# Optimization experiments

Measured on AMD Instinct MI355X. Metric: run time of the kernel, lower is better.

The kernel has to match this reference:

```python
import jax, jax.numpy as jnp
import numpy as np

SIZES = [128, 64, 32, 16, 8]   # H=W per pyramid level
REFINE = 2                     # gather/refine level -> 32x32
C = 256
GROUPS = 32                    # dim_out // 8
EPS = 1e-5


def _maxpool(x, k):
    # exact adaptive_max_pool2d when input size is divisible by output size
    if k == 1:
        return x
    return jax.lax.reduce_window(x, -jnp.inf, jax.lax.max,
                                 (1, 1, k, k), (1, 1, k, k), 'VALID')


def _upsample(x, f):
    # nearest-neighbor interpolate with exact integer scale factor
    if f == 1:
        return x
    return jnp.repeat(jnp.repeat(x, f, axis=2), f, axis=3)


def _conv1x1(x, w, b):
    return jnp.einsum('nchw,oc->nohw', x, w) + b[None, :, None, None]


def _group_norm(x, gamma, beta):
    n, c, h, w = x.shape
    xg = x.reshape(n, GROUPS, c // GROUPS, h, w)
    mu = xg.mean(axis=(2, 3, 4), keepdims=True)
    var = xg.var(axis=(2, 3, 4), keepdims=True)
    xg = (xg - mu) * jax.lax.rsqrt(var + EPS)
    return xg.reshape(n, c, h, w) * gamma[None, :, None, None] + beta[None, :, None, None]


def _nonlocal(x, g_w, g_b, th_w, th_b, ph_w, ph_b, out_w, out_b, gn_g, gn_b):
    n, c, h, w = x.shape
    N = h * w
    g_x = _conv1x1(x, g_w, g_b).reshape(n, c, N)       # [n,c,N]
    th_x = _conv1x1(x, th_w, th_b).reshape(n, c, N)
    ph_x = _conv1x1(x, ph_w, ph_b).reshape(n, c, N)
    # pairwise = theta^T @ phi / N  (dot_product mode, no softmax)
    pw = jnp.einsum('nci,ncj->nij', th_x, ph_x) / N    # [n,N,N]
    y = jnp.einsum('nij,ncj->nci', pw, g_x)            # [n,c,N]
    y = y.reshape(n, c, h, w)
    out = _group_norm(_conv1x1(y, out_w, out_b), gn_g, gn_b)
    return x + out


def reference(f0, f1, f2, f3, f4,
              g_w, g_b, th_w, th_b, ph_w, ph_b,
              out_w, out_b, gn_g, gn_b):
    feats = [f0, f1, f2, f3, f4]
    gs = SIZES[REFINE]
    gathered = []
    for i, f in enumerate(feats):
        if i < REFINE:
            gathered.append(_maxpool(f, SIZES[i] // gs))
        else:
            gathered.append(_upsample(f, gs // SIZES[i]))
    bsf = sum(gathered) / len(gathered)
    bsf = _nonlocal(bsf, g_w, g_b, th_w, th_b, ph_w, ph_b, out_w, out_b, gn_g, gn_b)
    outs = []
    for i, f in enumerate(feats):
        if i < REFINE:
            res = _upsample(bsf, SIZES[i] // gs)
        else:
            res = _maxpool(bsf, gs // SIZES[i])
        outs.append(res + f)
    return tuple(outs)


def setup_inputs() -> dict:
    key = jax.random.key(0)
    ks = jax.random.split(key, 16)
    inp = {}
    for i, s in enumerate(SIZES):
        inp[f'f{i}'] = jax.random.normal(ks[i], (4, C, s, s), dtype=jnp.float32)
    std = 0.01
    inp['g_w'] = jax.random.normal(ks[5], (C, C), dtype=jnp.float32) * std
    inp['g_b'] = jnp.zeros((C,), jnp.float32)
    inp['th_w'] = jax.random.normal(ks[6], (C, C), dtype=jnp.float32) * std
    inp['th_b'] = jnp.zeros((C,), jnp.float32)
    inp['ph_w'] = jax.random.normal(ks[7], (C, C), dtype=jnp.float32) * std
    inp['ph_b'] = jnp.zeros((C,), jnp.float32)
    inp['out_w'] = jax.random.normal(ks[8], (C, C), dtype=jnp.float32) * std
    inp['out_b'] = jnp.zeros((C,), jnp.float32)
    inp['gn_g'] = jnp.ones((C,), jnp.float32)
    inp['gn_b'] = jnp.zeros((C,), jnp.float32)
    return inp
```

## Files before the change

kernel.cpp:

```cpp
#include <hip/hip_runtime.h>

typedef __bf16 bf16x8 __attribute__((ext_vector_type(8)));
typedef float f32x4 __attribute__((ext_vector_type(4)));

#define OFF_BSF   0x000000
#define OFF_BSFT  0x400000
#define OFF_BSFB  0x600000
#define OFF_YT    0x600000
#define OFF_Z     0x800000
#define OFF_SBH   0xC00000
#define OFF_SBL   0xC80000
#define OFF_T0    0xD00000
#define OFF_OWB   0xE00000
#define OFF_GWT   0xE20000
#define OFF_PHT   0xE40000
#define OFF_THT   0xE60000
#define OFF_UB    0xE80000
#define OFF_VB    0xEA0000
#define OFF_UT    0xEC0000
#define OFF_RPART 0xEE0000
#define OFF_R     0xEF0000
#define OFF_UV    0xEF1000
#define OFF_V2P   0xEF1400
#define OFF_W2P   0xEF2400
#define OFF_S2    0xEF3400
#define OFF_CVEC  0xEF4000
#define OFF_STATS 0xEF9000
#define OFF_W2SP  0xEFA000

__global__ __launch_bounds__(256) void prep_k(
    const float* __restrict__ f0, const float* __restrict__ f1,
    const float* __restrict__ f2, const float* __restrict__ f3,
    const float* __restrict__ f4,
    const float* __restrict__ g_w, const float* __restrict__ ph_w,
    const float* __restrict__ th_w, const float* __restrict__ ow_w,
    const float* __restrict__ g_b, const float* __restrict__ ph_b,
    const float* __restrict__ th_b,
    char* __restrict__ ws)
{
  const int blk = blockIdx.x, t = threadIdx.x;
  __shared__ __attribute__((aligned(16))) union {
    __bf16 Lt[64][66];
    __bf16 T[64][72];
    float vec2[544];
  } sm;

  if (blk < 256) {
    float*  bsf   = (float*)(ws + OFF_BSF);
    __bf16* bsfT  = (__bf16*)(ws + OFF_BSFT);
    __bf16* bsfB  = (__bf16*)(ws + OFF_BSFB);
    float*  rpart = (float*)(ws + OFF_RPART);
    const int sblk = blk & 15, cblk = (blk >> 4) & 3, b = blk >> 6;
    const int c0 = cblk * 64, s0 = sblk * 64;
    const int spl = t & 63, sp = s0 + spl;
    const int y = sp >> 5, x = sp & 31;
#pragma unroll
    for (int i = 0; i < 16; ++i) {
      const int cl = (t >> 6) + i * 4;
      const int nc = b * 256 + c0 + cl;

      const float* p0 = f0 + (size_t)nc * 16384 + (y * 4) * 128 + x * 4;
      float4 r0 = *(const float4*)(p0);
      float4 r1 = *(const float4*)(p0 + 128);
      float4 r2 = *(const float4*)(p0 + 256);
      float4 r3 = *(const float4*)(p0 + 384);
      float a  = fmaxf(fmaxf(r0.x, r0.y), fmaxf(r0.z, r0.w));
      float bb = fmaxf(fmaxf(r1.x, r1.y), fmaxf(r1.z, r1.w));
      float c  = fmaxf(fmaxf(r2.x, r2.y), fmaxf(r2.z, r2.w));
      float d  = fmaxf(fmaxf(r3.x, r3.y), fmaxf(r3.z, r3.w));
      float m0v = fmaxf(fmaxf(a, bb), fmaxf(c, d));

      const float* p1 = f1 + (size_t)nc * 4096 + (y * 2) * 64 + x * 2;
      float2 s0v = *(const float2*)(p1);
      float2 s1v = *(const float2*)(p1 + 64);
      float m1v = fmaxf(fmaxf(s0v.x, s0v.y), fmaxf(s1v.x, s1v.y));

      float v2 = f2[(size_t)nc * 1024 + sp];
      float v3 = f3[(size_t)nc * 256 + (y >> 1) * 16 + (x >> 1)];
      float v4 = f4[(size_t)nc * 64  + (y >> 2) * 8  + (x >> 2)];
      float val = (m0v + m1v + v2 + v3 + v4) * 0.2f;
      bsf[(size_t)nc * 1024 + sp]  = val;
      bsfB[(size_t)nc * 1024 + sp] = (__bf16)val;
      sm.Lt[cl][spl] = (__bf16)val;
      float rs = val;
#pragma unroll
      for (int off = 32; off; off >>= 1) rs += __shfl_down(rs, off);
      if (spl == 0) rpart[sblk * 1024 + nc] = rs;
    }
    __syncthreads();
#pragma unroll
    for (int i = 0; i < 16; ++i) {
      int linear = t + i * 256;
      int spl2 = linear >> 6, cl2 = linear & 63;
      bsfT[((size_t)b * 1024 + s0 + spl2) * 256 + c0 + cl2] = sm.Lt[cl2][spl2];
    }
  } else if (blk < 304) {
    const int w = (blk - 256) >> 4, tl = (blk - 256) & 15;
    const float* src = (w == 0) ? g_w : (w == 1) ? ph_w : th_w;
    __bf16* dst = (__bf16*)(ws + ((w == 0) ? OFF_GWT : (w == 1) ? OFF_PHT : OFF_THT));
    const int ti = (tl >> 2) * 64, tj = (tl & 3) * 64;
#pragma unroll
    for (int i = 0; i < 4; ++i) {
      int idx = i * 256 + t;
      int r = idx >> 4, c4 = (idx & 15) << 2;
      float4 v = *(const float4*)&src[(size_t)(ti + r) * 256 + tj + c4];
      sm.T[c4 + 0][r] = (__bf16)v.x;
      sm.T[c4 + 1][r] = (__bf16)v.y;
      sm.T[c4 + 2][r] = (__bf16)v.z;
      sm.T[c4 + 3][r] = (__bf16)v.w;
    }
    __syncthreads();
#pragma unroll
    for (int i = 0; i < 2; ++i) {
      int idx = i * 256 + t;
      int aa = idx >> 3, cc = (idx & 7) << 3;
      bf16x8 o = *(const bf16x8*)&sm.T[aa][cc];
      *(bf16x8*)&dst[(size_t)(tj + aa) * 256 + ti + cc] = o;
    }
  } else if (blk < 308) {
    const int r0 = (blk - 304) * 64;
    __bf16* owB = (__bf16*)(ws + OFF_OWB);
#pragma unroll
    for (int i = 0; i < 8; ++i) {
      int lin = i * 2048 + t * 8;
      size_t gidx = (size_t)r0 * 256 + lin;
      float4 v0 = *(const float4*)&ow_w[gidx];
      float4 v1 = *(const float4*)&ow_w[gidx + 4];
      bf16x8 o;
      o[0] = (__bf16)v0.x; o[1] = (__bf16)v0.y; o[2] = (__bf16)v0.z; o[3] = (__bf16)v0.w;
      o[4] = (__bf16)v1.x; o[5] = (__bf16)v1.y; o[6] = (__bf16)v1.z; o[7] = (__bf16)v1.w;
      *(bf16x8*)&owB[gidx] = o;
    }
  } else if (blk < 324) {
    const int q = blk - 308;
    const int r0 = q * 16;
    float* uv = (float*)(ws + OFF_UV);
    sm.vec2[t] = g_b[t];
    __syncthreads();
    const int rl = t >> 4;
    const int ci = (t & 15) * 16;
    const float* p = ow_w + (size_t)(r0 + rl) * 256 + ci;
    float acc = 0.f;
#pragma unroll
    for (int u = 0; u < 4; ++u) {
      float4 v = *(const float4*)(p + u * 4);
      acc += v.x * sm.vec2[ci + u * 4]     + v.y * sm.vec2[ci + u * 4 + 1]
           + v.z * sm.vec2[ci + u * 4 + 2] + v.w * sm.vec2[ci + u * 4 + 3];
    }
    __syncthreads();
    sm.vec2[256 + rl * 17 + (t & 15)] = acc;
    __syncthreads();
    if (t < 16) {
      float s = 0.f;
#pragma unroll
      for (int i = 0; i < 16; ++i) s += sm.vec2[256 + t * 17 + i];
      uv[r0 + t] = s;
    }
  } else if (blk < 328) {
    const int q = blk - 324, c0 = q * 64;
    float* v2p = (float*)(ws + OFF_V2P);
    if (t < 64) sm.vec2[t] = th_b[c0 + t];
    __syncthreads();
    float acc = 0.f;
#pragma unroll 8
    for (int c = 0; c < 64; ++c)
      acc += ph_w[(size_t)(c0 + c) * 256 + t] * sm.vec2[c];
    v2p[q * 256 + t] = acc;
  } else if (blk < 332) {
    const int q = blk - 328, c0 = q * 64;
    float* w2p = (float*)(ws + OFF_W2P);
    if (t < 64) sm.vec2[t] = ph_b[c0 + t];
    __syncthreads();
    float acc = 0.f;
#pragma unroll 8
    for (int c = 0; c < 64; ++c)
      acc += th_w[(size_t)(c0 + c) * 256 + t] * sm.vec2[c];
    w2p[q * 256 + t] = acc;
  } else if (blk == 332) {
    float* s2 = (float*)(ws + OFF_S2);
    if (t < 64) {
      float pa = ph_b[t] * th_b[t] + ph_b[64 + t] * th_b[64 + t]
               + ph_b[128 + t] * th_b[128 + t] + ph_b[192 + t] * th_b[192 + t];
#pragma unroll
      for (int off = 32; off; off >>= 1) pa += __shfl_down(pa, off);
      if (t == 0) s2[0] = pa;
    }
    ((float*)(ws + OFF_STATS))[t] = 0.f;
  } else {
    float* cvec = (float*)(ws + OFF_CVEC);
#pragma unroll
    for (int i = 0; i < 4; ++i) cvec[i * 256 + t] = 0.f;
  }
}

__device__ __forceinline__ void gemm_acc(
    const __bf16* __restrict__ A, const __bf16* __restrict__ B,
    const int K, const int m0, const int n0,
    __bf16 (*Al)[64][72], __bf16 (*Bl)[64][72],
    f32x4 acc[2][2])
{
  const int t = threadIdx.x;
  const int lane = t & 63, wv = t >> 6;
  const int wm = (wv & 1) * 32, wn = (wv >> 1) * 32;
  const int fr = lane & 15, lk = (lane >> 4) * 8;
  const int sr = t >> 2, sk = (t & 3) * 16;

  const __bf16* Ar = A + (size_t)(m0 + sr) * K + sk;
  const __bf16* Br = B + (size_t)(n0 + sr) * K + sk;

  bf16x8 ra0 = *(const bf16x8*)(Ar);
  bf16x8 ra1 = *(const bf16x8*)(Ar + 8);
  bf16x8 rb0 = *(const bf16x8*)(Br);
  bf16x8 rb1 = *(const bf16x8*)(Br + 8);

  const int nIter = K >> 6;
  int p = 0;
  for (int it = 0; it < nIter; ++it) {
    *(bf16x8*)&Al[p][sr][sk]     = ra0;
    *(bf16x8*)&Al[p][sr][sk + 8] = ra1;
    *(bf16x8*)&Bl[p][sr][sk]     = rb0;
    *(bf16x8*)&Bl[p][sr][sk + 8] = rb1;
    __syncthreads();
    if (it + 1 < nIter) {
      const __bf16* An = Ar + (size_t)(it + 1) * 64;
      const __bf16* Bn = Br + (size_t)(it + 1) * 64;
      ra0 = *(const bf16x8*)(An);
      ra1 = *(const bf16x8*)(An + 8);
      rb0 = *(const bf16x8*)(Bn);
      rb1 = *(const bf16x8*)(Bn + 8);
    }
#pragma unroll
    for (int kk = 0; kk < 64; kk += 32) {
      bf16x8 a0 = *(const bf16x8*)&Al[p][wm + fr][kk + lk];
      bf16x8 a1 = *(const bf16x8*)&Al[p][wm + 16 + fr][kk + lk];
      bf16x8 b0 = *(const bf16x8*)&Bl[p][wn + fr][kk + lk];
      bf16x8 b1 = *(const bf16x8*)&Bl[p][wn + 16 + fr][kk + lk];
      acc[0][0] = __builtin_amdgcn_mfma_f32_16x16x32_bf16(a0, b0, acc[0][0], 0, 0, 0);
      acc[0][1] = __builtin_amdgcn_mfma_f32_16x16x32_bf16(a0, b1, acc[0][1], 0, 0, 0);
      acc[1][0] = __builtin_amdgcn_mfma_f32_16x16x32_bf16(a1, b0, acc[1][0], 0, 0, 0);
      acc[1][1] = __builtin_amdgcn_mfma_f32_16x16x32_bf16(a1, b1, acc[1][1], 0, 0, 0);
    }
    __syncthreads();
    p ^= 1;
  }
}

__device__ __forceinline__ void store_bf16(
    __bf16* dst, int ldst, const f32x4 acc[2][2],
    int m0, int n0, int wm, int wn, int rbase, int fr)
{
#pragma unroll
  for (int i = 0; i < 2; ++i)
#pragma unroll
    for (int r = 0; r < 4; ++r) {
      int m = m0 + wm + i * 16 + rbase + r;
#pragma unroll
      for (int j = 0; j < 2; ++j) {
        int n = n0 + wn + j * 16 + fr;
        dst[(size_t)m * ldst + n] = (__bf16)acc[i][j][r];
      }
    }
}

#define ZERO_ACC(acc) \
  _Pragma("unroll") for (int i_ = 0; i_ < 2; ++i_) \
  _Pragma("unroll") for (int j_ = 0; j_ < 2; ++j_) \
    acc[i_][j_] = (f32x4){0.f, 0.f, 0.f, 0.f};

__global__ __launch_bounds__(256) void p0_k(char* __restrict__ ws)
{
  const int blk = blockIdx.x, t = threadIdx.x;
  __shared__ __attribute__((aligned(16))) __bf16 Al[2][64][72];
  __shared__ __attribute__((aligned(16))) __bf16 Bl[2][64][72];
  float* shf = (float*)(&Al[0][0][0]);

  const int lane = t & 63, wv = t >> 6;
  const int wm = (wv & 1) * 32, wn = (wv >> 1) * 32;
  const int fr = lane & 15, rbase = (lane >> 4) * 4;
  (void)lane; (void)wv;

  const __bf16* bsfB = (const __bf16*)(ws + OFF_BSFB);

  if (blk < 64) {
    const int b = blk >> 4, tl = blk & 15;
    const int m0 = (tl >> 2) * 64, n0 = (tl & 3) * 64;
    f32x4 acc[2][2]; ZERO_ACC(acc);
    gemm_acc(bsfB + (size_t)b * 262144, bsfB + (size_t)b * 262144,
             1024, m0, n0, Al, Bl, acc);
    __bf16* oh = (__bf16*)(ws + OFF_SBH) + (size_t)b * 65536;
    __bf16* ol = (__bf16*)(ws + OFF_SBL) + (size_t)b * 65536;
#pragma unroll
    for (int i = 0; i < 2; ++i)
#pragma unroll
      for (int r = 0; r < 4; ++r) {
        int m = m0 + wm + i * 16 + rbase + r;
#pragma unroll
        for (int j = 0; j < 2; ++j) {
          int n = n0 + wn + j * 16 + fr;
          float v = acc[i][j][r];
          __bf16 h = (__bf16)v;
          oh[(size_t)m * 256 + n] = h;
          ol[(size_t)m * 256 + n] = (__bf16)(v - (float)h);
        }
      }
  } else if (blk < 80) {
    const int tl = blk - 64;
    const int m0 = (tl >> 2) * 64, n0 = (tl & 3) * 64;
    f32x4 acc[2][2]; ZERO_ACC(acc);
    gemm_acc((const __bf16*)(ws + OFF_OWB), (const __bf16*)(ws + OFF_GWT),
             256, m0, n0, Al, Bl, acc);
    __bf16* ub = (__bf16*)(ws + OFF_UB);
    __bf16* ut = (__bf16*)(ws + OFF_UT);
#pragma unroll
    for (int i = 0; i < 2; ++i)
#pragma unroll
      for (int r = 0; r < 4; ++r) {
        int m = m0 + wm + i * 16 + rbase + r;
#pragma unroll
        for (int j = 0; j < 2; ++j) {
          int n = n0 + wn + j * 16 + fr;
          __bf16 v = (__bf16)acc[i][j][r];
          ub[(size_t)m * 256 + n] = v;
          ut[(size_t)n * 256 + m] = v;
        }
      }
  } else if (blk < 96) {
    const int tl = blk - 80;
    const int m0 = (tl >> 2) * 64, n0 = (tl & 3) * 64;
    f32x4 acc[2][2]; ZERO_ACC(acc);
    gemm_acc((const __bf16*)(ws + OFF_PHT), (const __bf16*)(ws + OFF_THT),
             256, m0, n0, Al, Bl, acc);
    store_bf16((__bf16*)(ws + OFF_VB), 256, acc, m0, n0, wm, wn, rbase, fr);
  } else if (blk == 96) {
    const float* rpart = (const float*)(ws + OFF_RPART);
    float* Rr = (float*)(ws + OFF_R);
#pragma unroll
    for (int j2 = 0; j2 < 4; ++j2) {
      int idx = t + j2 * 256;
      float s = 0.f;
#pragma unroll
      for (int k = 0; k < 16; ++k) s += rpart[k * 1024 + idx];
      Rr[idx] = s;
    }
  } else {
    const int q = blk - 97;
    const int half = q >> 4, idx = q & 15;
    const int b = idx >> 2, seg = (idx & 3) * 256;
    const int ch0 = half * 128;
    const float* w2p = (const float*)(ws + OFF_W2P);
    const float* bsf = (const float*)(ws + OFF_BSF);
    float* w2sp = (float*)(ws + OFF_W2SP);
    if (t < 128) {
      int c = ch0 + t;
      shf[t] = w2p[c] + w2p[256 + c] + w2p[512 + c] + w2p[768 + c];
    }
    __syncthreads();
    float acc = 0.f;
#pragma unroll 8
    for (int c = 0; c < 128; ++c)
      acc += shf[c] * bsf[((size_t)(b * 256 + ch0 + c)) * 1024 + seg + t];
    w2sp[half * 4096 + b * 1024 + seg + t] = acc;
  }
}

__global__ __launch_bounds__(256) void p1_k(char* __restrict__ ws)
{
  const int blk = blockIdx.x, t = threadIdx.x;
  __shared__ __attribute__((aligned(16))) __bf16 Al[2][64][72];
  __shared__ __attribute__((aligned(16))) __bf16 Bl[2][64][72];
  float* shf = (float*)(&Al[0][0][0]);

  const int lane = t & 63, wv = t >> 6;
  const int wm = (wv & 1) * 32, wn = (wv >> 1) * 32;
  const int fr = lane & 15, rbase = (lane >> 4) * 4;
  (void)lane; (void)wv;

  const __bf16* UB = (const __bf16*)(ws + OFF_UB);
  const float* Rr  = (const float*)(ws + OFF_R);
  const float* uv  = (const float*)(ws + OFF_UV);

  if (blk < 64) {
    const int b = blk >> 4, tl = blk & 15;
    const int m0 = (tl >> 2) * 64, n0 = (tl & 3) * 64;
    f32x4 acc[2][2]; ZERO_ACC(acc);
    gemm_acc(UB, (const __bf16*)(ws + OFF_SBH) + (size_t)b * 65536,
             256, m0, n0, Al, Bl, acc);
    gemm_acc(UB, (const __bf16*)(ws + OFF_SBL) + (size_t)b * 65536,
             256, m0, n0, Al, Bl, acc);
    shf[t] = Rr[b * 256 + t];
    __syncthreads();
    __bf16* od = (__bf16*)(ws + OFF_T0) + (size_t)b * 65536;
#pragma unroll
    for (int i = 0; i < 2; ++i)
#pragma unroll
      for (int r = 0; r < 4; ++r) {
        int m = m0 + wm + i * 16 + rbase + r;
        float uvm = uv[m];
#pragma unroll
        for (int j = 0; j < 2; ++j) {
          int n = n0 + wn + j * 16 + fr;
          od[(size_t)m * 256 + n] = (__bf16)(acc[i][j][r] + uvm * shf[n]);
        }
      }
  } else if (blk < 320) {
    const int q = blk - 64;
    const int b = q >> 6, tl = q & 63;
    const int m0 = (tl >> 2) * 64, n0 = (tl & 3) * 64;
    f32x4 acc[2][2]; ZERO_ACC(acc);
    gemm_acc((const __bf16*)(ws + OFF_BSFT) + (size_t)b * 262144,
             (const __bf16*)(ws + OFF_VB), 256, m0, n0, Al, Bl, acc);
    const float* v2p = (const float*)(ws + OFF_V2P);
    shf[t] = v2p[t] + v2p[256 + t] + v2p[512 + t] + v2p[768 + t];
    __syncthreads();
    __bf16* od = (__bf16*)(ws + OFF_YT) + (size_t)b * 262144;
#pragma unroll
    for (int i = 0; i < 2; ++i)
#pragma unroll
      for (int r = 0; r < 4; ++r) {
        int m = m0 + wm + i * 16 + rbase + r;
#pragma unroll
        for (int j = 0; j < 2; ++j) {
          int n = n0 + wn + j * 16 + fr;
          od[(size_t)m * 256 + n] = (__bf16)(acc[i][j][r] + shf[n]);
        }
      }
  } else {
    const int q = blk - 320;
    const int b = q >> 2, cc = (q & 3) * 64;
    const __bf16* UT = (const __bf16*)(ws + OFF_UT);
    float* cvec = (float*)(ws + OFF_CVEC);
    if (t < 64) shf[t] = Rr[b * 256 + cc + t];
    __syncthreads();
    float acc = 0.f;
#pragma unroll 8
    for (int c = 0; c < 64; ++c)
      acc += (float)UT[(size_t)(cc + c) * 256 + t] * shf[c];
    atomicAdd(&cvec[b * 256 + t], acc);
  }
}

__global__ __launch_bounds__(256) void p2_k(char* __restrict__ ws,
                                            const float* __restrict__ ow_b)
{
  const int blk = blockIdx.x, t = threadIdx.x;
  __shared__ __attribute__((aligned(16))) __bf16 Al[2][64][72];
  __shared__ __attribute__((aligned(16))) __bf16 Bl[2][64][72];
  float* shf = (float*)(&Al[0][0][0]);

  const int lane = t & 63, wv = t >> 6;
  const int wm = (wv & 1) * 32, wn = (wv >> 1) * 32;
  const int fr = lane & 15, rbase = (lane >> 4) * 4;

  const int b = blk >> 6, t6 = blk & 63;
  const int mt = t6 >> 4, nt = t6 & 15;
  const int m0 = mt * 64, n0 = nt * 64;
  (void)nt;

  f32x4 acc[2][2]; ZERO_ACC(acc);
  gemm_acc((const __bf16*)(ws + OFF_T0) + (size_t)b * 65536,
           (const __bf16*)(ws + OFF_YT) + (size_t)b * 262144,
           256, m0, n0, Al, Bl, acc);

  const float* uv   = (const float*)(ws + OFF_UV);
  const float* cvec = (const float*)(ws + OFF_CVEC);
  const float* w2sp = (const float*)(ws + OFF_W2SP);
  const float s2v   = *(const float*)(ws + OFF_S2);
  float* SRAW = (float*)(ws + OFF_STATS);
  float* zb = (float*)(ws + OFF_Z) + (size_t)b * 262144;

  float gs[2] = {0.f, 0.f}, gq[2] = {0.f, 0.f};
  int gidx[2];
  const float s1024 = 1.f / 1024.f;
#pragma unroll
  for (int i = 0; i < 2; ++i) {
    gidx[i] = (wm + i * 16 + rbase) >> 3;
#pragma unroll
    for (int r = 0; r < 4; ++r) {
      int m = m0 + wm + i * 16 + rbase + r;
      float coefm = uv[m] + cvec[b * 256 + m] * s1024;
      float qm = s2v * coefm + ow_b[m];
#pragma unroll
      for (int j = 0; j < 2; ++j) {
        int n = n0 + wn + j * 16 + fr;
        float w2n = w2sp[b * 1024 + n] + w2sp[4096 + b * 1024 + n];
        float v = acc[i][j][r] * s1024 + coefm * w2n + qm;
        zb[(size_t)m * 1024 + n] = v;
        gs[i] += v;
        gq[i] += v * v;
      }
    }
  }
  __syncthreads();
  if (t < 16) shf[t] = 0.f;
  __syncthreads();
#pragma unroll
  for (int i = 0; i < 2; ++i) {
    atomicAdd(&shf[gidx[i] * 2], gs[i]);
    atomicAdd(&shf[gidx[i] * 2 + 1], gq[i]);
  }
  __syncthreads();
  if (t < 16) {
    int g = mt * 8 + (t >> 1);
    atomicAdd(&SRAW[(b * 32 + g) * 2 + (t & 1)], shf[t]);
  }
}

__device__ __forceinline__ float4 gmix(float4 bz, float4 zz, float a, float c)
{
  float4 r;
  r.x = bz.x + zz.x * a + c;
  r.y = bz.y + zz.y * a + c;
  r.z = bz.z + zz.z * a + c;
  r.w = bz.w + zz.w * a + c;
  return r;
}
__device__ __forceinline__ float max4(float4 v)
{ return fmaxf(fmaxf(v.x, v.y), fmaxf(v.z, v.w)); }

__device__ __forceinline__ void gn_coeff(const float2* __restrict__ ST,
                                         const float* __restrict__ gamma,
                                         const float* __restrict__ beta,
                                         int b, int ch, float& a, float& c0)
{
  float2 sq = ST[b * 32 + (ch >> 3)];
  float mean = sq.x * (1.0f / 8192.0f);
  float var  = sq.y * (1.0f / 8192.0f) - mean * mean;
  float inv  = rsqrtf(var + 1e-5f);
  a  = inv * gamma[ch];
  c0 = beta[ch] - mean * a;
}

__global__ __launch_bounds__(256) void scat_k(
    const char* __restrict__ ws,
    const float* __restrict__ f0, const float* __restrict__ f1,
    const float* __restrict__ f2, const float* __restrict__ f3,
    const float* __restrict__ f4,
    const float* __restrict__ gamma, const float* __restrict__ beta,
    float* __restrict__ out)
{
  const float* Z = (const float*)(ws + OFF_Z);
  const float* BSF = (const float*)(ws + OFF_BSF);
  const float2* ST = (const float2*)(ws + OFF_STATS);
  const int i4 = blockIdx.x * 256 + threadIdx.x;

  if (i4 < 4194304) {
    const int l = i4 << 2;
    const int x = l & 127, yy = (l >> 7) & 127, nc = l >> 14;
    const int ch = nc & 255, b = nc >> 8;
    float a, c0; gn_coeff(ST, gamma, beta, b, ch, a, c0);
    size_t base = (size_t)nc * 1024 + ((yy >> 2) << 5) + (x >> 2);
    float v = BSF[base] + Z[base] * a + c0;
    float4 f = ((const float4*)f0)[i4];
    float4 o; o.x = f.x + v; o.y = f.y + v; o.z = f.z + v; o.w = f.w + v;
    ((float4*)out)[i4] = o;
  } else if (i4 < 5242880) {
    const int l4 = i4 - 4194304;
    const int l = l4 << 2;
    const int x = l & 63, yy = (l >> 6) & 63, nc = l >> 12;
    const int ch = nc & 255, b = nc >> 8;
    float a, c0; gn_coeff(ST, gamma, beta, b, ch, a, c0);
    size_t base = (size_t)nc * 1024 + ((yy >> 1) << 5) + (x >> 1);
    float v0 = BSF[base] + Z[base] * a + c0;
    float v1 = BSF[base + 1] + Z[base + 1] * a + c0;
    float4 f = ((const float4*)f1)[l4];
    float4 o; o.x = f.x + v0; o.y = f.y + v0; o.z = f.z + v1; o.w = f.w + v1;
    ((float4*)out)[i4] = o;
  } else if (i4 < 5505024) {
    const int l4 = i4 - 5242880;
    const int l = l4 << 2;
    const int nc = l >> 10, e = l & 1023;
    const int ch = nc & 255, b = nc >> 8;
    float a, c0; gn_coeff(ST, gamma, beta, b, ch, a, c0);
    size_t base = (size_t)nc * 1024 + e;
    float4 z4 = *(const float4*)&Z[base];
    float4 b4 = *(const float4*)&BSF[base];
    float4 v = gmix(b4, z4, a, c0);
    float4 f = ((const float4*)f2)[l4];
    float4 o; o.x = f.x + v.x; o.y = f.y + v.y; o.z = f.z + v.z; o.w = f.w + v.w;
    ((float4*)out)[i4] = o;
  } else if (i4 < 5570560) {
    const int l4 = i4 - 5505024;
    const int l = l4 << 2;
    const int x = l & 15, yy = (l >> 4) & 15, nc = l >> 8;
    const int ch = nc & 255, b = nc >> 8;
    float a, c0; gn_coeff(ST, gamma, beta, b, ch, a, c0);
    size_t base = (size_t)nc * 1024;
    const int p0 = (yy * 2) * 32 + (x * 2);
    float4 r0a = gmix(*(const float4*)&BSF[base + p0],      *(const float4*)&Z[base + p0],      a, c0);
    float4 r0b = gmix(*(const float4*)&BSF[base + p0 + 4],  *(const float4*)&Z[base + p0 + 4],  a, c0);
    float4 r1a = gmix(*(const float4*)&BSF[base + p0 + 32], *(const float4*)&Z[base + p0 + 32], a, c0);
    float4 r1b = gmix(*(const float4*)&BSF[base + p0 + 36], *(const float4*)&Z[base + p0 + 36], a, c0);
    float4 f = ((const float4*)f3)[l4];
    float4 o;
    o.x = f.x + fmaxf(fmaxf(r0a.x, r0a.y), fmaxf(r1a.x, r1a.y));
    o.y = f.y + fmaxf(fmaxf(r0a.z, r0a.w), fmaxf(r1a.z, r1a.w));
    o.z = f.z + fmaxf(fmaxf(r0b.x, r0b.y), fmaxf(r1b.x, r1b.y));
    o.w = f.w + fmaxf(fmaxf(r0b.z, r0b.w), fmaxf(r1b.z, r1b.w));
    ((float4*)out)[i4] = o;
  } else {
    const int l4 = i4 - 5570560;
    const int l = l4 << 2;
    const int x = l & 7, yy = (l >> 3) & 7, nc = l >> 6;
    const int ch = nc & 255, b = nc >> 8;
    float a, c0; gn_coeff(ST, gamma, beta, b, ch, a, c0);
    size_t base = (size_t)nc * 1024;
    float4 mx = {-3.4e38f, -3.4e38f, -3.4e38f, -3.4e38f};
#pragma unroll
    for (int r = 0; r < 4; ++r) {
      const float* zp = &Z[base + (size_t)(yy * 4 + r) * 32 + x * 4];
      const float* bp = &BSF[base + (size_t)(yy * 4 + r) * 32 + x * 4];
      float4 q0 = gmix(*(const float4*)(bp),      *(const float4*)(zp),      a, c0);
      float4 q1 = gmix(*(const float4*)(bp + 4),  *(const float4*)(zp + 4),  a, c0);
      float4 q2 = gmix(*(const float4*)(bp + 8),  *(const float4*)(zp + 8),  a, c0);
      float4 q3 = gmix(*(const float4*)(bp + 12), *(const float4*)(zp + 12), a, c0);
      mx.x = fmaxf(mx.x, max4(q0));
      mx.y = fmaxf(mx.y, max4(q1));
      mx.z = fmaxf(mx.z, max4(q2));
      mx.w = fmaxf(mx.w, max4(q3));
    }
    float4 f = ((const float4*)f4)[l4];
    float4 o; o.x = f.x + mx.x; o.y = f.y + mx.y; o.z = f.z + mx.z; o.w = f.w + mx.w;
    ((float4*)out)[i4] = o;
  }
}

extern "C" void kernel_launch(void* const* d_in, const int* in_sizes, int n_in,
                              void* d_out, int out_size, void* d_ws, size_t ws_size,
                              hipStream_t stream)
{
  (void)in_sizes; (void)n_in; (void)out_size; (void)ws_size;
  const float* f0   = (const float*)d_in[0];
  const float* f1   = (const float*)d_in[1];
  const float* f2   = (const float*)d_in[2];
  const float* f3   = (const float*)d_in[3];
  const float* f4   = (const float*)d_in[4];
  const float* g_w  = (const float*)d_in[5];
  const float* g_b  = (const float*)d_in[6];
  const float* th_w = (const float*)d_in[7];
  const float* th_b = (const float*)d_in[8];
  const float* ph_w = (const float*)d_in[9];
  const float* ph_b = (const float*)d_in[10];
  const float* ow_w = (const float*)d_in[11];
  const float* ow_b = (const float*)d_in[12];
  const float* gn_g = (const float*)d_in[13];
  const float* gn_b = (const float*)d_in[14];
  char* ws = (char*)d_ws;

  prep_k<<<334, 256, 0, stream>>>(f0, f1, f2, f3, f4,
                                  g_w, ph_w, th_w, ow_w,
                                  g_b, ph_b, th_b, ws);
  p0_k<<<129, 256, 0, stream>>>(ws);
  p1_k<<<336, 256, 0, stream>>>(ws);
  p2_k<<<256, 256, 0, stream>>>(ws, ow_b);
  scat_k<<<21824, 256, 0, stream>>>(ws, f0, f1, f2, f3, f4, gn_g, gn_b,
                                    (float*)d_out);
}
```

Before: 87.84 us.

## Compute weight-product matrices in prep kernel and rebalance stages across kernels

The weight-only products (out_w·g_w into UB/UT and ph_w^T·th_w into VB) move out of a separate bf16-cast-then-MFMA stage and into the prep kernel. There they are computed directly in fp32 FMA from LDS, which removes the intermediate bf16 weight buffers. Work is then redistributed: the bsf^T·V GEMM, the w2sp reduction and the cvec blocks move into p0 alongside the sbh/sbl split, and p1 keeps only the 64 UB·S GEMM tiles. The R reduction is recomputed inline from rpart instead of being materialised. This shortens the dependency chain across kernels, but it adds scalar FMA work (16 blocks each doing 256×16×256) to prep, which could lengthen that kernel.

```diff
diff --git a/kernel.cpp b/kernel.cpp
--- a/kernel.cpp
+++ b/kernel.cpp
@@ -6,20 +6,14 @@
 #define OFF_BSF   0x000000
 #define OFF_BSFT  0x400000
 #define OFF_BSFB  0x600000
-#define OFF_YT    0x600000
 #define OFF_Z     0x800000
 #define OFF_SBH   0xC00000
 #define OFF_SBL   0xC80000
 #define OFF_T0    0xD00000
-#define OFF_OWB   0xE00000
-#define OFF_GWT   0xE20000
-#define OFF_PHT   0xE40000
-#define OFF_THT   0xE60000
 #define OFF_UB    0xE80000
 #define OFF_VB    0xEA0000
 #define OFF_UT    0xEC0000
 #define OFF_RPART 0xEE0000
-#define OFF_R     0xEF0000
 #define OFF_UV    0xEF1000
 #define OFF_V2P   0xEF1400
 #define OFF_W2P   0xEF2400
@@ -27,6 +21,7 @@
 #define OFF_CVEC  0xEF4000
 #define OFF_STATS 0xEF9000
 #define OFF_W2SP  0xEFA000
+#define OFF_YT    0xF10000
 
 __global__ __launch_bounds__(256) void prep_k(
     const float* __restrict__ f0, const float* __restrict__ f1,
@@ -41,7 +36,7 @@
   const int blk = blockIdx.x, t = threadIdx.x;
   __shared__ __attribute__((aligned(16))) union {
     __bf16 Lt[64][66];
-    __bf16 T[64][72];
+    float wk[4096];
     float vec2[544];
   } sm;
 
@@ -94,45 +89,56 @@
       int spl2 = linear >> 6, cl2 = linear & 63;
       bsfT[((size_t)b * 1024 + s0 + spl2) * 256 + c0 + cl2] = sm.Lt[cl2][spl2];
     }
+  } else if (blk < 272) {
+    const int q = blk - 256, m0 = q * 16;
+#pragma unroll
+    for (int i = 0; i < 16; ++i) {
+      int lin = t + i * 256;
+      int row = lin >> 8, k = lin & 255;
+      sm.wk[row * 256 + k] = ow_w[(size_t)(m0 + row) * 256 + k];
+    }
+    __syncthreads();
+    float acc[16];
+#pragma unroll
+    for (int mi = 0; mi < 16; ++mi) acc[mi] = 0.f;
+    for (int k = 0; k < 256; ++k) {
+      float gv = g_w[(size_t)k * 256 + t];
+#pragma unroll
+      for (int mi = 0; mi < 16; ++mi) acc[mi] += sm.wk[mi * 256 + k] * gv;
+    }
+    __bf16* ub = (__bf16*)(ws + OFF_UB);
+    __bf16* ut = (__bf16*)(ws + OFF_UT);
+#pragma unroll
+    for (int mi = 0; mi < 16; ++mi)
+      ub[(size_t)(m0 + mi) * 256 + t] = (__bf16)acc[mi];
+    bf16x8 o0, o1;
+#pragma unroll
+    for (int j = 0; j < 8; ++j) { o0[j] = (__bf16)acc[j]; o1[j] = (__bf16)acc[8 + j]; }
+    *(bf16x8*)&ut[(size_t)t * 256 + m0]     = o0;
+    *(bf16x8*)&ut[(size_t)t * 256 + m0 + 8] = o1;
+  } else if (blk < 288) {
+    const int q = blk - 272, m0 = q * 16;
+#pragma unroll
+    for (int i = 0; i < 16; ++i) {
+      int lin = t + i * 256;
+      int k = lin >> 4, mi = lin & 15;
+      sm.wk[k * 16 + mi] = ph_w[(size_t)k * 256 + m0 + mi];
+    }
+    __syncthreads();
+    float acc[16];
+#pragma unroll
+    for (int mi = 0; mi < 16; ++mi) acc[mi] = 0.f;
+    for (int k = 0; k < 256; ++k) {
+      float tv = th_w[(size_t)k * 256 + t];
+#pragma unroll
+      for (int mi = 0; mi < 16; ++mi) acc[mi] += sm.wk[k * 16 + mi] * tv;
+    }
+    __bf16* vb = (__bf16*)(ws + OFF_VB);
+#pragma unroll
+    for (int mi = 0; mi < 16; ++mi)
+      vb[(size_t)(m0 + mi) * 256 + t] = (__bf16)acc[mi];
   } else if (blk < 304) {
-    const int w = (blk - 256) >> 4, tl = (blk - 256) & 15;
-    const float* src = (w == 0) ? g_w : (w == 1) ? ph_w : th_w;
-    __bf16* dst = (__bf16*)(ws + ((w == 0) ? OFF_GWT : (w == 1) ? OFF_PHT : OFF_THT));
-    const int ti = (tl >> 2) * 64, tj = (tl & 3) * 64;
-#pragma unroll
-    for (int i = 0; i < 4; ++i) {
-      int idx = i * 256 + t;
-      int r = idx >> 4, c4 = (idx & 15) << 2;
-      float4 v = *(const float4*)&src[(size_t)(ti + r) * 256 + tj + c4];
-      sm.T[c4 + 0][r] = (__bf16)v.x;
-      sm.T[c4 + 1][r] = (__bf16)v.y;
-      sm.T[c4 + 2][r] = (__bf16)v.z;
-      sm.T[c4 + 3][r] = (__bf16)v.w;
-    }
-    __syncthreads();
-#pragma unroll
-    for (int i = 0; i < 2; ++i) {
-      int idx = i * 256 + t;
-      int aa = idx >> 3, cc = (idx & 7) << 3;
-      bf16x8 o = *(const bf16x8*)&sm.T[aa][cc];
-      *(bf16x8*)&dst[(size_t)(tj + aa) * 256 + ti + cc] = o;
-    }
-  } else if (blk < 308) {
-    const int r0 = (blk - 304) * 64;
-    __bf16* owB = (__bf16*)(ws + OFF_OWB);
-#pragma unroll
-    for (int i = 0; i < 8; ++i) {
-      int lin = i * 2048 + t * 8;
-      size_t gidx = (size_t)r0 * 256 + lin;
-      float4 v0 = *(const float4*)&ow_w[gidx];
-      float4 v1 = *(const float4*)&ow_w[gidx + 4];
-      bf16x8 o;
-      o[0] = (__bf16)v0.x; o[1] = (__bf16)v0.y; o[2] = (__bf16)v0.z; o[3] = (__bf16)v0.w;
-      o[4] = (__bf16)v1.x; o[5] = (__bf16)v1.y; o[6] = (__bf16)v1.z; o[7] = (__bf16)v1.w;
-      *(bf16x8*)&owB[gidx] = o;
-    }
-  } else if (blk < 324) {
-    const int q = blk - 308;
+    const int q = blk - 288;
     const int r0 = q * 16;
     float* uv = (float*)(ws + OFF_UV);
     sm.vec2[t] = g_b[t];
@@ -156,8 +162,8 @@
       for (int i = 0; i < 16; ++i) s += sm.vec2[256 + t * 17 + i];
       uv[r0 + t] = s;
     }
-  } else if (blk < 328) {
-    const int q = blk - 324, c0 = q * 64;
+  } else if (blk < 308) {
+    const int q = blk - 304, c0 = q * 64;
     float* v2p = (float*)(ws + OFF_V2P);
     if (t < 64) sm.vec2[t] = th_b[c0 + t];
     __syncthreads();
@@ -166,8 +172,8 @@
     for (int c = 0; c < 64; ++c)
       acc += ph_w[(size_t)(c0 + c) * 256 + t] * sm.vec2[c];
     v2p[q * 256 + t] = acc;
-  } else if (blk < 332) {
-    const int q = blk - 328, c0 = q * 64;
+  } else if (blk < 312) {
+    const int q = blk - 308, c0 = q * 64;
     float* w2p = (float*)(ws + OFF_W2P);
     if (t < 64) sm.vec2[t] = ph_b[c0 + t];
     __syncthreads();
@@ -176,7 +182,7 @@
     for (int c = 0; c < 64; ++c)
       acc += th_w[(size_t)(c0 + c) * 256 + t] * sm.vec2[c];
     w2p[q * 256 + t] = acc;
-  } else if (blk == 332) {
+  } else if (blk == 312) {
     float* s2 = (float*)(ws + OFF_S2);
     if (t < 64) {
       float pa = ph_b[t] * th_b[t] + ph_b[64 + t] * th_b[64 + t]
@@ -245,23 +251,6 @@
   }
 }
 
-__device__ __forceinline__ void store_bf16(
-    __bf16* dst, int ldst, const f32x4 acc[2][2],
-    int m0, int n0, int wm, int wn, int rbase, int fr)
-{
-#pragma unroll
-  for (int i = 0; i < 2; ++i)
-#pragma unroll
-    for (int r = 0; r < 4; ++r) {
-      int m = m0 + wm + i * 16 + rbase + r;
-#pragma unroll
-      for (int j = 0; j < 2; ++j) {
-        int n = n0 + wn + j * 16 + fr;
-        dst[(size_t)m * ldst + n] = (__bf16)acc[i][j][r];
-      }
-    }
-}
-
 #define ZERO_ACC(acc) \
   _Pragma("unroll") for (int i_ = 0; i_ < 2; ++i_) \
   _Pragma("unroll") for (int j_ = 0; j_ < 2; ++j_) \
@@ -280,6 +269,7 @@
   (void)lane; (void)wv;
 
   const __bf16* bsfB = (const __bf16*)(ws + OFF_BSFB);
+  const float* rpart = (const float*)(ws + OFF_RPART);
 
   if (blk < 64) {
     const int b = blk >> 4, tl = blk & 15;
@@ -301,105 +291,6 @@
           __bf16 h = (__bf16)v;
           oh[(size_t)m * 256 + n] = h;
           ol[(size_t)m * 256 + n] = (__bf16)(v - (float)h);
-        }
-      }
-  } else if (blk < 80) {
-    const int tl = blk - 64;
-    const int m0 = (tl >> 2) * 64, n0 = (tl & 3) * 64;
-    f32x4 acc[2][2]; ZERO_ACC(acc);
-    gemm_acc((const __bf16*)(ws + OFF_OWB), (const __bf16*)(ws + OFF_GWT),
-             256, m0, n0, Al, Bl, acc);
-    __bf16* ub = (__bf16*)(ws + OFF_UB);
-    __bf16* ut = (__bf16*)(ws + OFF_UT);
-#pragma unroll
-    for (int i = 0; i < 2; ++i)
-#pragma unroll
-      for (int r = 0; r < 4; ++r) {
-        int m = m0 + wm + i * 16 + rbase + r;
-#pragma unroll
-        for (int j = 0; j < 2; ++j) {
-          int n = n0 + wn + j * 16 + fr;
-          __bf16 v = (__bf16)acc[i][j][r];
-          ub[(size_t)m * 256 + n] = v;
-          ut[(size_t)n * 256 + m] = v;
-        }
-      }
-  } else if (blk < 96) {
-    const int tl = blk - 80;
-    const int m0 = (tl >> 2) * 64, n0 = (tl & 3) * 64;
-    f32x4 acc[2][2]; ZERO_ACC(acc);
-    gemm_acc((const __bf16*)(ws + OFF_PHT), (const __bf16*)(ws + OFF_THT),
-             256, m0, n0, Al, Bl, acc);
-    store_bf16((__bf16*)(ws + OFF_VB), 256, acc, m0, n0, wm, wn, rbase, fr);
-  } else if (blk == 96) {
-    const float* rpart = (const float*)(ws + OFF_RPART);
-    float* Rr = (float*)(ws + OFF_R);
-#pragma unroll
-    for (int j2 = 0; j2 < 4; ++j2) {
-      int idx = t + j2 * 256;
-      float s = 0.f;
-#pragma unroll
-      for (int k = 0; k < 16; ++k) s += rpart[k * 1024 + idx];
-      Rr[idx] = s;
-    }
-  } else {
-    const int q = blk - 97;
-    const int half = q >> 4, idx = q & 15;
-    const int b = idx >> 2, seg = (idx & 3) * 256;
-    const int ch0 = half * 128;
-    const float* w2p = (const float*)(ws + OFF_W2P);
-    const float* bsf = (const float*)(ws + OFF_BSF);
-    float* w2sp = (float*)(ws + OFF_W2SP);
-    if (t < 128) {
-      int c = ch0 + t;
-      shf[t] = w2p[c] + w2p[256 + c] + w2p[512 + c] + w2p[768 + c];
-    }
-    __syncthreads();
-    float acc = 0.f;
-#pragma unroll 8
-    for (int c = 0; c < 128; ++c)
-      acc += shf[c] * bsf[((size_t)(b * 256 + ch0 + c)) * 1024 + seg + t];
-    w2sp[half * 4096 + b * 1024 + seg + t] = acc;
-  }
-}
-
-__global__ __launch_bounds__(256) void p1_k(char* __restrict__ ws)
-{
-  const int blk = blockIdx.x, t = threadIdx.x;
-  __shared__ __attribute__((aligned(16))) __bf16 Al[2][64][72];
-  __shared__ __attribute__((aligned(16))) __bf16 Bl[2][64][72];
-  float* shf = (float*)(&Al[0][0][0]);
-
-  const int lane = t & 63, wv = t >> 6;
-  const int wm = (wv & 1) * 32, wn = (wv >> 1) * 32;
-  const int fr = lane & 15, rbase = (lane >> 4) * 4;
-  (void)lane; (void)wv;
-
-  const __bf16* UB = (const __bf16*)(ws + OFF_UB);
-  const float* Rr  = (const float*)(ws + OFF_R);
-  const float* uv  = (const float*)(ws + OFF_UV);
-
-  if (blk < 64) {
-    const int b = blk >> 4, tl = blk & 15;
-    const int m0 = (tl >> 2) * 64, n0 = (tl & 3) * 64;
-    f32x4 acc[2][2]; ZERO_ACC(acc);
-    gemm_acc(UB, (const __bf16*)(ws + OFF_SBH) + (size_t)b * 65536,
-             256, m0, n0, Al, Bl, acc);
-    gemm_acc(UB, (const __bf16*)(ws + OFF_SBL) + (size_t)b * 65536,
-             256, m0, n0, Al, Bl, acc);
-    shf[t] = Rr[b * 256 + t];
-    __syncthreads();
-    __bf16* od = (__bf16*)(ws + OFF_T0) + (size_t)b * 65536;
-#pragma unroll
-    for (int i = 0; i < 2; ++i)
-#pragma unroll
-      for (int r = 0; r < 4; ++r) {
-        int m = m0 + wm + i * 16 + rbase + r;
-        float uvm = uv[m];
-#pragma unroll
-        for (int j = 0; j < 2; ++j) {
-          int n = n0 + wn + j * 16 + fr;
-          od[(size_t)m * 256 + n] = (__bf16)(acc[i][j][r] + uvm * shf[n]);
         }
       }
   } else if (blk < 320) {
@@ -424,12 +315,35 @@
           od[(size_t)m * 256 + n] = (__bf16)(acc[i][j][r] + shf[n]);
         }
       }
+  } else if (blk < 352) {
+    const int q = blk - 320;
+    const int half = q >> 4, idx = q & 15;
+    const int b = idx >> 2, seg = (idx & 3) * 256;
+    const int ch0 = half * 128;
+    const float* w2p = (const float*)(ws + OFF_W2P);
+    const float* bsf = (const float*)(ws + OFF_BSF);
+    float* w2sp = (float*)(ws + OFF_W2SP);
+    if (t < 128) {
+      int c = ch0 + t;
+      shf[t] = w2p[c] + w2p[256 + c] + w2p[512 + c] + w2p[768 + c];
+    }
+    __syncthreads();
+    float acc = 0.f;
+#pragma unroll 8
+    for (int c = 0; c < 128; ++c)
+      acc += shf[c] * bsf[((size_t)(b * 256 + ch0 + c)) * 1024 + seg + t];
+    w2sp[half * 4096 + b * 1024 + seg + t] = acc;
   } else {
-    const int q = blk - 320;
+    const int q = blk - 352;
     const int b = q >> 2, cc = (q & 3) * 64;
     const __bf16* UT = (const __bf16*)(ws + OFF_UT);
     float* cvec = (float*)(ws + OFF_CVEC);
-    if (t < 64) shf[t] = Rr[b * 256 + cc + t];
+    if (t < 64) {
+      float s = 0.f;
+#pragma unroll
+      for (int k = 0; k < 16; ++k) s += rpart[k * 1024 + b * 256 + cc + t];
+      shf[t] = s;
+    }
     __syncthreads();
     float acc = 0.f;
 #pragma unroll 8
@@ -437,6 +351,49 @@
       acc += (float)UT[(size_t)(cc + c) * 256 + t] * shf[c];
     atomicAdd(&cvec[b * 256 + t], acc);
   }
+}
+
+__global__ __launch_bounds__(256) void p1_k(char* __restrict__ ws)
+{
+  const int blk = blockIdx.x, t = threadIdx.x;
+  __shared__ __attribute__((aligned(16))) __bf16 Al[2][64][72];
+  __shared__ __attribute__((aligned(16))) __bf16 Bl[2][64][72];
+  float* shf = (float*)(&Al[0][0][0]);
+
+  const int lane = t & 63, wv = t >> 6;
+  const int wm = (wv & 1) * 32, wn = (wv >> 1) * 32;
+  const int fr = lane & 15, rbase = (lane >> 4) * 4;
+  (void)lane; (void)wv;
+
+  const __bf16* UB = (const __bf16*)(ws + OFF_UB);
+  const float* uv  = (const float*)(ws + OFF_UV);
+  const float* rpart = (const float*)(ws + OFF_RPART);
+
+  const int b = blk >> 4, tl = blk & 15;
+  const int m0 = (tl >> 2) * 64, n0 = (tl & 3) * 64;
+  f32x4 acc[2][2]; ZERO_ACC(acc);
+  gemm_acc(UB, (const __bf16*)(ws + OFF_SBH) + (size_t)b * 65536,
+           256, m0, n0, Al, Bl, acc);
+  gemm_acc(UB, (const __bf16*)(ws + OFF_SBL) + (size_t)b * 65536,
+           256, m0, n0, Al, Bl, acc);
+  float s = 0.f;
+#pragma unroll
+  for (int k = 0; k < 16; ++k) s += rpart[k * 1024 + b * 256 + t];
+  shf[t] = s;
+  __syncthreads();
+  __bf16* od = (__bf16*)(ws + OFF_T0) + (size_t)b * 65536;
+#pragma unroll
+  for (int i = 0; i < 2; ++i)
+#pragma unroll
+    for (int r = 0; r < 4; ++r) {
+      int m = m0 + wm + i * 16 + rbase + r;
+      float uvm = uv[m];
+#pragma unroll
+      for (int j = 0; j < 2; ++j) {
+        int n = n0 + wn + j * 16 + fr;
+        od[(size_t)m * 256 + n] = (__bf16)(acc[i][j][r] + uvm * shf[n]);
+      }
+    }
 }
 
 __global__ __launch_bounds__(256) void p2_k(char* __restrict__ ws,
@@ -646,11 +603,11 @@
   const float* gn_b = (const float*)d_in[14];
   char* ws = (char*)d_ws;
 
-  prep_k<<<334, 256, 0, stream>>>(f0, f1, f2, f3, f4,
+  prep_k<<<314, 256, 0, stream>>>(f0, f1, f2, f3, f4,
                                   g_w, ph_w, th_w, ow_w,
                                   g_b, ph_b, th_b, ws);
-  p0_k<<<129, 256, 0, stream>>>(ws);
-  p1_k<<<336, 256, 0, stream>>>(ws);
+  p0_k<<<368, 256, 0, stream>>>(ws);
+  p1_k<<<64, 256, 0, stream>>>(ws);
   p2_k<<<256, 256, 0, stream>>>(ws, ow_b);
   scat_k<<<21824, 256, 0, stream>>>(ws, f0, f1, f2, f3, f4, gn_g, gn_b,
                                     (float*)d_out);
```

Result: slower. 103.3 us (+17.6%).
